# Performance work log

Measured on AMD Instinct MI355X. Metric: run time of the kernel, lower is better.

The kernel has to match this reference:

```python
import jax, jax.numpy as jnp
import numpy as np

DIM = 1024
HEADS = 16
GROUPS = 4
DIM_HEAD = 64
INNER = HEADS * DIM_HEAD  # 1024
KV_DIM = 2 * DIM_HEAD * GROUPS  # 512
B, N = 4, 2048
EPS = 1e-6


def _layernorm(x, scale, bias, eps=EPS):
    mu = jnp.mean(x, axis=-1, keepdims=True)
    var = jnp.mean(jnp.square(x - mu), axis=-1, keepdims=True)
    return (x - mu) * jax.lax.rsqrt(var + eps) * scale + bias


def setup_inputs() -> dict:
    key = jax.random.key(0)
    ks = jax.random.split(key, 10)
    lecun = lambda k, shape: jax.random.normal(k, shape, jnp.float32) * (1.0 / np.sqrt(shape[0]))
    return {
        "x": jax.random.normal(ks[0], (B, N, DIM), jnp.float32),
        "ln_scale": jnp.ones((DIM,), jnp.float32),
        "ln_bias": jnp.zeros((DIM,), jnp.float32),
        "Wq": lecun(ks[1], (DIM, INNER)),
        "Wkv": lecun(ks[2], (DIM, KV_DIM)),
        "qn_scale": jnp.ones((DIM_HEAD,), jnp.float32),
        "qn_bias": jnp.zeros((DIM_HEAD,), jnp.float32),
        "kn_scale": jnp.ones((DIM_HEAD,), jnp.float32),
        "kn_bias": jnp.zeros((DIM_HEAD,), jnp.float32),
        "Wout": lecun(ks[3], (INNER, DIM)),
    }


def reference(x, ln_scale, ln_bias, Wq, Wkv, qn_scale, qn_bias, kn_scale, kn_bias, Wout):
    b, n, _ = x.shape
    g, hg, d = GROUPS, HEADS // GROUPS, DIM_HEAD
    scale = d ** -0.5
    xn = _layernorm(x, ln_scale, ln_bias)
    # q: (b,n,inner) -> (b,h,n,d)
    q = (xn @ Wq).reshape(b, n, HEADS, d).transpose(0, 2, 1, 3)
    kv = xn @ Wkv
    k, v = jnp.split(kv, 2, axis=-1)
    # (b,n,g*d) -> (b,g,n,d)
    k = k.reshape(b, n, g, d).transpose(0, 2, 1, 3)
    v = v.reshape(b, n, g, d).transpose(0, 2, 1, 3)
    q = _layernorm(q, qn_scale, qn_bias)
    k = _layernorm(k, kn_scale, kn_bias)
    # split heads into groups: (b, g*hg, n, d) -> (b, g, hg, n, d)
    qg = q.reshape(b, g, hg, n, d)
    dots = jnp.einsum('bghqd,bgkd->bghqk', qg, k) * scale
    attn = jax.nn.softmax(dots, axis=-1)
    out = jnp.einsum('bghqk,bgkd->bghqd', attn, v)  # (b,g,hg,n,d)
    out = out.transpose(0, 3, 1, 2, 4).reshape(b, n, g * hg * d)
    return out @ Wout
```

## Files before the change

### kernel.cpp

```cpp
#include <hip/hip_runtime.h>
#include <cstdint>
#include <cstddef>

typedef unsigned short u16;
typedef __attribute__((ext_vector_type(4))) float f32x4;
typedef __attribute__((ext_vector_type(8))) __bf16 bf16x8;
typedef __attribute__((ext_vector_type(4))) __bf16 bf16x4;
typedef __attribute__((ext_vector_type(8))) unsigned short u16x8;
typedef __attribute__((ext_vector_type(4))) unsigned short u16x4;

#define DEV static __device__ __forceinline__

#if __has_builtin(__builtin_amdgcn_exp2f)
#define EXP2(x) __builtin_amdgcn_exp2f(x)
#else
#define EXP2(x) exp2f(x)
#endif

DEV float bf2f(u16 v) { return __uint_as_float(((unsigned)v) << 16); }
DEV u16 f2bf(float f) {
  unsigned u = __float_as_uint(f);
  return (u16)((u + 0x7FFFu + ((u >> 16) & 1u)) >> 16);
}

DEV void gl_lds16(const void* g, void* l) {
  __builtin_amdgcn_global_load_lds((const __attribute__((address_space(1))) void*)g,
                                   (__attribute__((address_space(3))) void*)l, 16, 0, 0);
}

__global__ __launch_bounds__(256) void transpose64(const float* __restrict__ in,
                                                   u16* __restrict__ out, int incols) {
  __shared__ __attribute__((aligned(16))) u16 t[64 * 72];
  const int r0 = blockIdx.x * 64, c0 = blockIdx.y * 64, tid = threadIdx.x;
#pragma unroll
  for (int i = 0; i < 2; i++) {
    int c = i * 256 + tid;
    int row = c >> 3, cc = c & 7;
    const float* src = &in[(size_t)(r0 + row) * incols + c0 + cc * 8];
    f32x4 v0 = *(const f32x4*)src;
    f32x4 v1 = *(const f32x4*)(src + 4);
    u16x8 o;
#pragma unroll
    for (int j = 0; j < 4; j++) { o[j] = f2bf(v0[j]); o[4 + j] = f2bf(v1[j]); }
    *(u16x8*)&t[row * 72 + cc * 8] = o;
  }
  __syncthreads();
#pragma unroll
  for (int i = 0; i < 2; i++) {
    int c = i * 256 + tid;
    int d = c >> 3, nc = c & 7;
    u16x8 o;
#pragma unroll
    for (int j = 0; j < 8; j++) o[j] = t[(nc * 8 + j) * 72 + d];
    *(u16x8*)&out[(size_t)(c0 + d) * 1024 + r0 + nc * 8] = o;
  }
}

__global__ __launch_bounds__(256) void ln_x(const float* __restrict__ x,
                                            const float* __restrict__ sc,
                                            const float* __restrict__ bi,
                                            u16* __restrict__ xn) {
  __shared__ float red[8];
  const int row = blockIdx.x, tid = threadIdx.x;
  const int w = tid >> 6;
  f32x4 f = *(const f32x4*)&x[(size_t)row * 1024 + tid * 4];
  float s = f[0] + f[1] + f[2] + f[3];
  float q = f[0] * f[0] + f[1] * f[1] + f[2] * f[2] + f[3] * f[3];
#pragma unroll
  for (int off = 1; off < 64; off <<= 1) {
    s += __shfl_xor(s, off);
    q += __shfl_xor(q, off);
  }
  if ((tid & 63) == 0) { red[w] = s; red[4 + w] = q; }
  __syncthreads();
  float S = red[0] + red[1] + red[2] + red[3];
  float Q = red[4] + red[5] + red[6] + red[7];
  float mu = S * (1.0f / 1024.0f);
  float var = Q * (1.0f / 1024.0f) - mu * mu;
  float rs = rsqrtf(var + 1e-6f);
  f32x4 scv = *(const f32x4*)&sc[tid * 4];
  f32x4 biv = *(const f32x4*)&bi[tid * 4];
  u16* o = xn + (size_t)row * 1024 + tid * 4;
#pragma unroll
  for (int j = 0; j < 4; j++) o[j] = f2bf((f[j] - mu) * rs * scv[j] + biv[j]);
}

template <bool F32OUT>
__global__ __launch_bounds__(256) void gemm_bt(const u16* __restrict__ A,
                                               const u16* __restrict__ Bt,
                                               void* __restrict__ Cp,
                                               int M, int N, int K) {
  __shared__ __attribute__((aligned(16))) u16 Als[128 * 64];
  __shared__ __attribute__((aligned(16))) u16 Bls[128 * 64];
  const int tid = threadIdx.x;
  const int w = tid >> 6, lane = tid & 63, ln = lane & 15, quad = lane >> 4;
  const int m0 = blockIdx.y * 128, n0 = blockIdx.x * 128;
  const int moff = (w & 1) * 64, noff = (w >> 1) * 64;
  const f32x4 fzero = {0.f, 0.f, 0.f, 0.f};
  f32x4 acc[4][4];
#pragma unroll
  for (int i = 0; i < 4; i++)
#pragma unroll
    for (int j = 0; j < 4; j++) acc[i][j] = fzero;

  const u16* aS[4];
  const u16* bS[4];
#pragma unroll
  for (int i = 0; i < 4; i++) {
    int s = i * 256 + tid;
    int row = s >> 3, cs = (s & 7) ^ (row & 7);
    aS[i] = A + (size_t)(m0 + row) * K + cs * 8;
    bS[i] = Bt + (size_t)(n0 + row) * K + cs * 8;
  }

  for (int k0 = 0; k0 < K; k0 += 64) {
    __syncthreads();
#pragma unroll
    for (int i = 0; i < 4; i++) {
      int s = i * 256 + tid;
      gl_lds16(aS[i] + k0, &Als[s * 8]);
      gl_lds16(bS[i] + k0, &Bls[s * 8]);
    }
    __syncthreads();
#pragma unroll
    for (int kk = 0; kk < 2; kk++) {
      bf16x8 af[4], bfv[4];
#pragma unroll
      for (int mi = 0; mi < 4; mi++)
        af[mi] = *(const bf16x8*)
            &Als[(moff + mi * 16 + ln) * 64 + (((kk * 4 + quad) ^ (ln & 7)) * 8)];
#pragma unroll
      for (int ni = 0; ni < 4; ni++)
        bfv[ni] = *(const bf16x8*)
            &Bls[(noff + ni * 16 + ln) * 64 + (((kk * 4 + quad) ^ (ln & 7)) * 8)];
#pragma unroll
      for (int mi = 0; mi < 4; mi++)
#pragma unroll
        for (int ni = 0; ni < 4; ni++)
          acc[mi][ni] = __builtin_amdgcn_mfma_f32_16x16x32_bf16(af[mi], bfv[ni],
                                                                acc[mi][ni], 0, 0, 0);
    }
  }
#pragma unroll
  for (int mi = 0; mi < 4; mi++)
#pragma unroll
    for (int ni = 0; ni < 4; ni++)
#pragma unroll
      for (int r = 0; r < 4; r++) {
        size_t m = m0 + moff + mi * 16 + quad * 4 + r;
        size_t n = n0 + noff + ni * 16 + ln;
        if (F32OUT)
          ((float*)Cp)[m * N + n] = acc[mi][ni][r];
        else
          ((u16*)Cp)[m * N + n] = f2bf(acc[mi][ni][r]);
      }
}

__global__ __launch_bounds__(256) void qk_ln(const u16* __restrict__ qkv,
                                             const float* __restrict__ qs,
                                             const float* __restrict__ qb,
                                             const float* __restrict__ ks,
                                             const float* __restrict__ kb,
                                             u16* __restrict__ Q,
                                             u16* __restrict__ Kb) {
  const float SCL = 0.18033688011112042f;
  const int m = blockIdx.x;
  const int b = m >> 11, n = m & 2047;
  const int tid = threadIdx.x, w = tid >> 6, lane = tid & 63;
  const u16* rowp = qkv + (size_t)m * 1536;
  const float qsc = qs[lane], qbi = qb[lane];
  const float ksc = ks[lane], kbi = kb[lane];
#pragma unroll
  for (int i = 0; i < 4; i++) {
    int h = w * 4 + i;
    float v = bf2f(rowp[h * 64 + lane]);
    float s = v, q2 = v * v;
#pragma unroll
    for (int off = 1; off < 64; off <<= 1) {
      s += __shfl_xor(s, off);
      q2 += __shfl_xor(q2, off);
    }
    float mu = s * (1.0f / 64.0f);
    float var = q2 * (1.0f / 64.0f) - mu * mu;
    float y = ((v - mu) * rsqrtf(var + 1e-6f) * qsc + qbi) * SCL;
    Q[((size_t)(b * 16 + h) * 2048 + n) * 64 + lane] = f2bf(y);
  }
  {
    int g = w;
    float v = bf2f(rowp[1024 + g * 64 + lane]);
    float s = v, q2 = v * v;
#pragma unroll
    for (int off = 1; off < 64; off <<= 1) {
      s += __shfl_xor(s, off);
      q2 += __shfl_xor(q2, off);
    }
    float mu = s * (1.0f / 64.0f);
    float var = q2 * (1.0f / 64.0f) - mu * mu;
    float y = (v - mu) * rsqrtf(var + 1e-6f) * ksc + kbi;
    Kb[((size_t)(b * 4 + g) * 2048 + n) * 64 + lane] = f2bf(y);
  }
}

__global__ __launch_bounds__(256) void vtrans(const u16* __restrict__ qkv,
                                              u16* __restrict__ Vt) {
  __shared__ __attribute__((aligned(16))) u16 t[64 * 72];
  const int n0 = blockIdx.x * 64;
  const int bg = blockIdx.y;
  const int b = bg >> 2, g = bg & 3;
  const int tid = threadIdx.x;
  const u16* src = qkv + (size_t)(b * 2048 + n0) * 1536 + 1280 + g * 64;
#pragma unroll
  for (int i = 0; i < 2; i++) {
    int c = i * 256 + tid;
    int row = c >> 3, cc = c & 7;
    *(f32x4*)&t[row * 72 + cc * 8] = *(const f32x4*)&src[(size_t)row * 1536 + cc * 8];
  }
  __syncthreads();
  u16* dst = Vt + (size_t)bg * 64 * 2048 + n0;
#pragma unroll
  for (int i = 0; i < 2; i++) {
    int c = i * 256 + tid;
    int d = c >> 3, nc = c & 7;
    const int pA = 32 * (nc >> 2) + (nc & 1) * 16 + ((nc >> 1) & 1) * 4;
    u16x8 o;
#pragma unroll
    for (int j = 0; j < 8; j++) o[j] = t[(nc * 8 + j) * 72 + d];
    u16x4 lo = {o[0], o[1], o[2], o[3]};
    u16x4 hi = {o[4], o[5], o[6], o[7]};
    *(u16x4*)&dst[(size_t)d * 2048 + pA] = lo;
    *(u16x4*)&dst[(size_t)d * 2048 + pA + 8] = hi;
  }
}

__global__ __launch_bounds__(128, 2) void attn(const u16* __restrict__ Q,
                                               const u16* __restrict__ Kb,
                                               const u16* __restrict__ Vt,
                                               u16* __restrict__ Out) {
  __shared__ __attribute__((aligned(16))) u16 Kls0[64 * 64];
  __shared__ __attribute__((aligned(16))) u16 Kls1[64 * 64];
  __shared__ __attribute__((aligned(16))) u16 Vls0[64 * 64];
  __shared__ __attribute__((aligned(16))) u16 Vls1[64 * 64];
  const int qt = blockIdx.x;
  const int bh = blockIdx.y;
  const int b = bh >> 4, h = bh & 15, g = h >> 2;
  const int tid = threadIdx.x, w = tid >> 6, lane = tid & 63;
  const int ln = lane & 15, quad = lane >> 4;
  const u16* Qg = Q + ((size_t)(b * 16 + h) * 2048 + qt * 128 + w * 64) * 64;
  const u16* Kg = Kb + (size_t)(b * 4 + g) * 2048 * 64;
  const u16* Vg = Vt + (size_t)(b * 4 + g) * 64 * 2048;
  const f32x4 fzero = {0.f, 0.f, 0.f, 0.f};

  bf16x8 qf[4][2];
#pragma unroll
  for (int mi = 0; mi < 4; mi++)
#pragma unroll
    for (int ks2 = 0; ks2 < 2; ks2++)
      qf[mi][ks2] = *(const bf16x8*)&Qg[(size_t)(mi * 16 + ln) * 64 + ks2 * 32 + quad * 8];

  f32x4 oacc[4][4];
#pragma unroll
  for (int ni = 0; ni < 4; ni++)
#pragma unroll
    for (int mi = 0; mi < 4; mi++) oacc[ni][mi] = fzero;
  float lacc[4] = {0.f, 0.f, 0.f, 0.f};

  int krow[4], kcs[4];
#pragma unroll
  for (int i = 0; i < 4; i++) {
    int s = i * 128 + tid;
    krow[i] = s >> 3;
    kcs[i] = (s & 7) ^ (krow[i] & 7);
  }

  auto STAGE = [&](int kt, u16* Kd, u16* Vd) {
#pragma unroll
    for (int i = 0; i < 4; i++) {
      int s = i * 128 + tid;
      gl_lds16(Kg + (size_t)(kt * 64 + krow[i]) * 64 + kcs[i] * 8, &Kd[s * 8]);
      gl_lds16(Vg + (size_t)krow[i] * 2048 + kt * 64 + kcs[i] * 8, &Vd[s * 8]);
    }
  };

  auto BODY = [&](int kt, const u16* K_, const u16* V_, u16* Kn, u16* Vn) {
    if (kt + 1 < 32) STAGE(kt + 1, Kn, Vn);

#pragma unroll
    for (int c = 0; c < 2; c++) {
      bf16x8 kf[2][2];
#pragma unroll
      for (int ni = 0; ni < 2; ni++) {
        const int kr = (c * 32 + ni * 16 + ln) * 64;
        kf[ni][0] = *(const bf16x8*)&K_[kr + ((quad ^ (ln & 7)) * 8)];
        kf[ni][1] = *(const bf16x8*)&K_[kr + (((4 + quad) ^ (ln & 7)) * 8)];
      }

      f32x4 sacc[4][2];
      __builtin_amdgcn_s_setprio(1);
#pragma unroll
      for (int ni = 0; ni < 2; ni++)
#pragma unroll
        for (int mi = 0; mi < 4; mi++) {
          f32x4 tt = __builtin_amdgcn_mfma_f32_16x16x32_bf16(kf[ni][0], qf[mi][0],
                                                             fzero, 0, 0, 0);
          sacc[mi][ni] = __builtin_amdgcn_mfma_f32_16x16x32_bf16(kf[ni][1], qf[mi][1],
                                                                 tt, 0, 0, 0);
        }
      __builtin_amdgcn_s_setprio(0);

      bf16x8 pfa[4];
#pragma unroll
      for (int mi = 0; mi < 4; mi++) {
        float p0 = EXP2(sacc[mi][0][0]);
        float p1 = EXP2(sacc[mi][0][1]);
        float p2 = EXP2(sacc[mi][0][2]);
        float p3 = EXP2(sacc[mi][0][3]);
        float p4 = EXP2(sacc[mi][1][0]);
        float p5 = EXP2(sacc[mi][1][1]);
        float p6 = EXP2(sacc[mi][1][2]);
        float p7 = EXP2(sacc[mi][1][3]);
        lacc[mi] += ((p0 + p1) + (p2 + p3)) + ((p4 + p5) + (p6 + p7));
        pfa[mi][0] = (__bf16)p0; pfa[mi][1] = (__bf16)p1;
        pfa[mi][2] = (__bf16)p2; pfa[mi][3] = (__bf16)p3;
        pfa[mi][4] = (__bf16)p4; pfa[mi][5] = (__bf16)p5;
        pfa[mi][6] = (__bf16)p6; pfa[mi][7] = (__bf16)p7;
      }

#pragma unroll
      for (int ni = 0; ni < 4; ni++) {
        bf16x8 vf = *(const bf16x8*)
            &V_[(ni * 16 + ln) * 64 + (((4 * c + quad) ^ (ln & 7)) * 8)];
        __builtin_amdgcn_s_setprio(1);
#pragma unroll
        for (int mi = 0; mi < 4; mi++)
          oacc[ni][mi] = __builtin_amdgcn_mfma_f32_16x16x32_bf16(vf, pfa[mi],
                                                                 oacc[ni][mi], 0, 0, 0);
        __builtin_amdgcn_s_setprio(0);
      }
    }
    __syncthreads();
  };

  STAGE(0, Kls0, Vls0);
  __syncthreads();
  for (int kt = 0; kt < 32; kt += 2) {
    BODY(kt, Kls0, Vls0, Kls1, Vls1);
    BODY(kt + 1, Kls1, Vls1, Kls0, Vls0);
  }

#pragma unroll
  for (int mi = 0; mi < 4; mi++) {
    float ls = lacc[mi];
    ls += __shfl_xor(ls, 16);
    ls += __shfl_xor(ls, 32);
    float inv = 1.0f / ls;
    u16* Og = Out + ((size_t)b * 2048 + qt * 128 + w * 64 + mi * 16 + ln) * 1024 + h * 64;
#pragma unroll
    for (int ni = 0; ni < 4; ni++) {
      bf16x4 ov = {(__bf16)(oacc[ni][mi][0] * inv), (__bf16)(oacc[ni][mi][1] * inv),
                   (__bf16)(oacc[ni][mi][2] * inv), (__bf16)(oacc[ni][mi][3] * inv)};
      *(bf16x4*)&Og[ni * 16 + quad * 4] = ov;
    }
  }
}

extern "C" void kernel_launch(void* const* d_in, const int* in_sizes, int n_in,
                              void* d_out, int out_size, void* d_ws, size_t ws_size,
                              hipStream_t stream) {
  const float* x    = (const float*)d_in[0];
  const float* lns  = (const float*)d_in[1];
  const float* lnb  = (const float*)d_in[2];
  const float* Wq   = (const float*)d_in[3];
  const float* Wkv  = (const float*)d_in[4];
  const float* qns  = (const float*)d_in[5];
  const float* qnb  = (const float*)d_in[6];
  const float* kns  = (const float*)d_in[7];
  const float* knb  = (const float*)d_in[8];
  const float* Wout = (const float*)d_in[9];
  float* out = (float*)d_out;
  char* ws = (char*)d_ws;

  const size_t o_xn  = 0;
  const size_t o_qkv = 16777216;
  const size_t o_bt  = o_qkv + 25165824;
  const size_t o_k   = o_bt + 3145728;
  const size_t o_vt  = o_k + 4194304;
  u16* xn   = (u16*)(ws + o_xn);
  u16* qkv  = (u16*)(ws + o_qkv);
  u16* bt   = (u16*)(ws + o_bt);
  u16* Kbuf = (u16*)(ws + o_k);
  u16* Vtb  = (u16*)(ws + o_vt);
  u16* Qbuf = xn;
  u16* aout = qkv;

  transpose64<<<dim3(16, 16), 256, 0, stream>>>(Wq, bt, 1024);
  transpose64<<<dim3(16, 8), 256, 0, stream>>>(Wkv, bt + 1024 * 1024, 512);
  ln_x<<<8192, 256, 0, stream>>>(x, lns, lnb, xn);
  gemm_bt<false><<<dim3(12, 64), 256, 0, stream>>>(xn, bt, qkv, 8192, 1536, 1024);
  transpose64<<<dim3(16, 16), 256, 0, stream>>>(Wout, bt, 1024);
  qk_ln<<<8192, 256, 0, stream>>>(qkv, qns, qnb, kns, knb, Qbuf, Kbuf);
  vtrans<<<dim3(32, 16), 256, 0, stream>>>(qkv, Vtb);
  attn<<<dim3(16, 64), 128, 0, stream>>>(Qbuf, Kbuf, Vtb, aout);
  gemm_bt<true><<<dim3(8, 64), 256, 0, stream>>>(aout, bt, out, 8192, 1024, 1024);

  (void)in_sizes; (void)n_in; (void)out_size; (void)ws_size;
}
```

Measured before the change: 272.3 us.

## Load K/V fragments directly from global in attention, drop LDS staging

The attention kernel no longer stages K and V tiles through double-buffered shared memory with barriers. Each wave now loads its MFMA fragments straight from global memory (relying on L2/L1 reuse) with a register-level K prefetch of the next chunk. Blocks grow to 256 threads with four waves of 32 query rows each, so per-wave accumulators shrink and occupancy can rise. The cost is more redundant global/cache traffic and exposed load latency per wave in place of shared-memory reuse and synchronisation.

```diff
diff --git a/kernel.cpp b/kernel.cpp
--- a/kernel.cpp
+++ b/kernel.cpp
@@ -232,128 +232,106 @@
   }
 }
 
-__global__ __launch_bounds__(128, 2) void attn(const u16* __restrict__ Q,
+__global__ __launch_bounds__(256, 3) void attn(const u16* __restrict__ Q,
                                                const u16* __restrict__ Kb,
                                                const u16* __restrict__ Vt,
                                                u16* __restrict__ Out) {
-  __shared__ __attribute__((aligned(16))) u16 Kls0[64 * 64];
-  __shared__ __attribute__((aligned(16))) u16 Kls1[64 * 64];
-  __shared__ __attribute__((aligned(16))) u16 Vls0[64 * 64];
-  __shared__ __attribute__((aligned(16))) u16 Vls1[64 * 64];
   const int qt = blockIdx.x;
   const int bh = blockIdx.y;
   const int b = bh >> 4, h = bh & 15, g = h >> 2;
   const int tid = threadIdx.x, w = tid >> 6, lane = tid & 63;
   const int ln = lane & 15, quad = lane >> 4;
-  const u16* Qg = Q + ((size_t)(b * 16 + h) * 2048 + qt * 128 + w * 64) * 64;
+  const u16* Qg = Q + ((size_t)(b * 16 + h) * 2048 + qt * 128 + w * 32) * 64;
   const u16* Kg = Kb + (size_t)(b * 4 + g) * 2048 * 64;
   const u16* Vg = Vt + (size_t)(b * 4 + g) * 64 * 2048;
   const f32x4 fzero = {0.f, 0.f, 0.f, 0.f};
 
-  bf16x8 qf[4][2];
-#pragma unroll
-  for (int mi = 0; mi < 4; mi++)
+  bf16x8 qf[2][2];
+#pragma unroll
+  for (int mi = 0; mi < 2; mi++)
 #pragma unroll
     for (int ks2 = 0; ks2 < 2; ks2++)
       qf[mi][ks2] = *(const bf16x8*)&Qg[(size_t)(mi * 16 + ln) * 64 + ks2 * 32 + quad * 8];
 
-  f32x4 oacc[4][4];
+  f32x4 oacc[4][2];
 #pragma unroll
   for (int ni = 0; ni < 4; ni++)
 #pragma unroll
-    for (int mi = 0; mi < 4; mi++) oacc[ni][mi] = fzero;
-  float lacc[4] = {0.f, 0.f, 0.f, 0.f};
-
-  int krow[4], kcs[4];
-#pragma unroll
-  for (int i = 0; i < 4; i++) {
-    int s = i * 128 + tid;
-    krow[i] = s >> 3;
-    kcs[i] = (s & 7) ^ (krow[i] & 7);
-  }
-
-  auto STAGE = [&](int kt, u16* Kd, u16* Vd) {
-#pragma unroll
-    for (int i = 0; i < 4; i++) {
-      int s = i * 128 + tid;
-      gl_lds16(Kg + (size_t)(kt * 64 + krow[i]) * 64 + kcs[i] * 8, &Kd[s * 8]);
-      gl_lds16(Vg + (size_t)krow[i] * 2048 + kt * 64 + kcs[i] * 8, &Vd[s * 8]);
-    }
+    for (int mi = 0; mi < 2; mi++) oacc[ni][mi] = fzero;
+  float lacc[2] = {0.f, 0.f};
+
+  const u16* Kl = Kg + (size_t)ln * 64 + quad * 8;
+  const u16* Vl = Vg + (size_t)ln * 2048 + quad * 8;
+
+#define LOADK(cc, kf)                                                          \
+  {                                                                            \
+    _Pragma("unroll") for (int ni = 0; ni < 2; ni++)                           \
+        _Pragma("unroll") for (int s = 0; s < 2; s++)                          \
+        kf[ni][s] = *(const bf16x8*)&Kl[(size_t)((cc) * 32 + ni * 16) * 64 + s * 32]; \
+  }
+
+  auto CHUNK = [&](int cc, const bf16x8 kf[2][2], bf16x8 kn[2][2]) {
+    bf16x8 vf[4];
+#pragma unroll
+    for (int ni = 0; ni < 4; ni++)
+      vf[ni] = *(const bf16x8*)&Vl[(size_t)ni * 16 * 2048 + cc * 32];
+    LOADK(cc + 1, kn);
+
+    f32x4 sacc[2][2];
+    __builtin_amdgcn_s_setprio(1);
+#pragma unroll
+    for (int ni = 0; ni < 2; ni++)
+#pragma unroll
+      for (int mi = 0; mi < 2; mi++) {
+        f32x4 tt = __builtin_amdgcn_mfma_f32_16x16x32_bf16(kf[ni][0], qf[mi][0],
+                                                           fzero, 0, 0, 0);
+        sacc[mi][ni] = __builtin_amdgcn_mfma_f32_16x16x32_bf16(kf[ni][1], qf[mi][1],
+                                                               tt, 0, 0, 0);
+      }
+    __builtin_amdgcn_s_setprio(0);
+
+    bf16x8 pfa[2];
+#pragma unroll
+    for (int mi = 0; mi < 2; mi++) {
+      float p0 = EXP2(sacc[mi][0][0]);
+      float p1 = EXP2(sacc[mi][0][1]);
+      float p2 = EXP2(sacc[mi][0][2]);
+      float p3 = EXP2(sacc[mi][0][3]);
+      float p4 = EXP2(sacc[mi][1][0]);
+      float p5 = EXP2(sacc[mi][1][1]);
+      float p6 = EXP2(sacc[mi][1][2]);
+      float p7 = EXP2(sacc[mi][1][3]);
+      lacc[mi] += ((p0 + p1) + (p2 + p3)) + ((p4 + p5) + (p6 + p7));
+      pfa[mi][0] = (__bf16)p0; pfa[mi][1] = (__bf16)p1;
+      pfa[mi][2] = (__bf16)p2; pfa[mi][3] = (__bf16)p3;
+      pfa[mi][4] = (__bf16)p4; pfa[mi][5] = (__bf16)p5;
+      pfa[mi][6] = (__bf16)p6; pfa[mi][7] = (__bf16)p7;
+    }
+
+    __builtin_amdgcn_s_setprio(1);
+#pragma unroll
+    for (int ni = 0; ni < 4; ni++)
+#pragma unroll
+      for (int mi = 0; mi < 2; mi++)
+        oacc[ni][mi] = __builtin_amdgcn_mfma_f32_16x16x32_bf16(vf[ni], pfa[mi],
+                                                               oacc[ni][mi], 0, 0, 0);
+    __builtin_amdgcn_s_setprio(0);
   };
 
-  auto BODY = [&](int kt, const u16* K_, const u16* V_, u16* Kn, u16* Vn) {
-    if (kt + 1 < 32) STAGE(kt + 1, Kn, Vn);
-
-#pragma unroll
-    for (int c = 0; c < 2; c++) {
-      bf16x8 kf[2][2];
-#pragma unroll
-      for (int ni = 0; ni < 2; ni++) {
-        const int kr = (c * 32 + ni * 16 + ln) * 64;
-        kf[ni][0] = *(const bf16x8*)&K_[kr + ((quad ^ (ln & 7)) * 8)];
-        kf[ni][1] = *(const bf16x8*)&K_[kr + (((4 + quad) ^ (ln & 7)) * 8)];
-      }
-
-      f32x4 sacc[4][2];
-      __builtin_amdgcn_s_setprio(1);
-#pragma unroll
-      for (int ni = 0; ni < 2; ni++)
-#pragma unroll
-        for (int mi = 0; mi < 4; mi++) {
-          f32x4 tt = __builtin_amdgcn_mfma_f32_16x16x32_bf16(kf[ni][0], qf[mi][0],
-                                                             fzero, 0, 0, 0);
-          sacc[mi][ni] = __builtin_amdgcn_mfma_f32_16x16x32_bf16(kf[ni][1], qf[mi][1],
-                                                                 tt, 0, 0, 0);
-        }
-      __builtin_amdgcn_s_setprio(0);
-
-      bf16x8 pfa[4];
-#pragma unroll
-      for (int mi = 0; mi < 4; mi++) {
-        float p0 = EXP2(sacc[mi][0][0]);
-        float p1 = EXP2(sacc[mi][0][1]);
-        float p2 = EXP2(sacc[mi][0][2]);
-        float p3 = EXP2(sacc[mi][0][3]);
-        float p4 = EXP2(sacc[mi][1][0]);
-        float p5 = EXP2(sacc[mi][1][1]);
-        float p6 = EXP2(sacc[mi][1][2]);
-        float p7 = EXP2(sacc[mi][1][3]);
-        lacc[mi] += ((p0 + p1) + (p2 + p3)) + ((p4 + p5) + (p6 + p7));
-        pfa[mi][0] = (__bf16)p0; pfa[mi][1] = (__bf16)p1;
-        pfa[mi][2] = (__bf16)p2; pfa[mi][3] = (__bf16)p3;
-        pfa[mi][4] = (__bf16)p4; pfa[mi][5] = (__bf16)p5;
-        pfa[mi][6] = (__bf16)p6; pfa[mi][7] = (__bf16)p7;
-      }
-
-#pragma unroll
-      for (int ni = 0; ni < 4; ni++) {
-        bf16x8 vf = *(const bf16x8*)
-            &V_[(ni * 16 + ln) * 64 + (((4 * c + quad) ^ (ln & 7)) * 8)];
-        __builtin_amdgcn_s_setprio(1);
-#pragma unroll
-        for (int mi = 0; mi < 4; mi++)
-          oacc[ni][mi] = __builtin_amdgcn_mfma_f32_16x16x32_bf16(vf, pfa[mi],
-                                                                 oacc[ni][mi], 0, 0, 0);
-        __builtin_amdgcn_s_setprio(0);
-      }
-    }
-    __syncthreads();
-  };
-
-  STAGE(0, Kls0, Vls0);
-  __syncthreads();
-  for (int kt = 0; kt < 32; kt += 2) {
-    BODY(kt, Kls0, Vls0, Kls1, Vls1);
-    BODY(kt + 1, Kls1, Vls1, Kls0, Vls0);
-  }
-
-#pragma unroll
-  for (int mi = 0; mi < 4; mi++) {
+  bf16x8 ka[2][2], kb_[2][2];
+  LOADK(0, ka);
+  for (int cc = 0; cc < 64; cc += 2) {
+    CHUNK(cc, ka, kb_);
+    CHUNK(cc + 1, kb_, ka);
+  }
+
+#pragma unroll
+  for (int mi = 0; mi < 2; mi++) {
     float ls = lacc[mi];
     ls += __shfl_xor(ls, 16);
     ls += __shfl_xor(ls, 32);
     float inv = 1.0f / ls;
-    u16* Og = Out + ((size_t)b * 2048 + qt * 128 + w * 64 + mi * 16 + ln) * 1024 + h * 64;
+    u16* Og = Out + ((size_t)b * 2048 + qt * 128 + w * 32 + mi * 16 + ln) * 1024 + h * 64;
 #pragma unroll
     for (int ni = 0; ni < 4; ni++) {
       bf16x4 ov = {(__bf16)(oacc[ni][mi][0] * inv), (__bf16)(oacc[ni][mi][1] * inv),
@@ -361,6 +339,7 @@
       *(bf16x4*)&Og[ni * 16 + quad * 4] = ov;
     }
   }
+#undef LOADK
 }
 
 extern "C" void kernel_launch(void* const* d_in, const int* in_sizes, int n_in,
@@ -399,7 +378,7 @@
   transpose64<<<dim3(16, 16), 256, 0, stream>>>(Wout, bt, 1024);
   qk_ln<<<8192, 256, 0, stream>>>(qkv, qns, qnb, kns, knb, Qbuf, Kbuf);
   vtrans<<<dim3(32, 16), 256, 0, stream>>>(qkv, Vtb);
-  attn<<<dim3(16, 64), 128, 0, stream>>>(Qbuf, Kbuf, Vtb, aout);
+  attn<<<dim3(16, 64), 256, 0, stream>>>(Qbuf, Kbuf, Vtb, aout);
   gemm_bt<true><<<dim3(8, 64), 256, 0, stream>>>(aout, bt, out, 8192, 1024, 1024);
 
   (void)in_sizes; (void)n_in; (void)out_size; (void)ws_size;
```

New measurement: 420.1 us. 54.3% more time.
